# Kernel optimization log

Measured on AMD Instinct MI355X. Metric: run time of the kernel, lower is better.

The kernel has to match this reference:

```python
import jax
import jax.numpy as jnp
import numpy as np
from jax import lax


def setup_inputs() -> dict:
    key = jax.random.key(0)
    k0, k1 = jax.random.split(key)
    B, C, H, W = 8, 256, 96, 96
    FM0 = jax.random.normal(k0, (B, C, H, W), dtype=jnp.float32)
    FM1 = jax.random.normal(k1, (B, C, H, W), dtype=jnp.float32)
    return {"FM0": FM0, "FM1": FM1, "d_max": 4, "stride": 1}


def pointwise_correlation(FM0, FM1, d_max, stride):
    """out[b,h,w,i,j] = sum_c FM0[b,c,h,w] * FM1[b,c,h+(i-d)*s, w+(j-d)*s],
    with zero padding outside FM1's spatial extent."""
    B, C, H, W = FM0.shape
    D = 2 * d_max + 1
    p = d_max * stride
    FM1p = jnp.pad(FM1, ((0, 0), (0, 0), (p, p), (p, p)))
    offs = jnp.arange(D, dtype=jnp.int32) * stride  # start offsets into padded map
    ys, xs = jnp.meshgrid(offs, offs, indexing="ij")
    offsets = jnp.stack([ys.ravel(), xs.ravel()], axis=-1)  # (D*D, 2)

    def step(carry, off):
        sl = lax.dynamic_slice(FM1p, (0, 0, off[0], off[1]), (B, C, H, W))
        corr = jnp.einsum("bchw,bchw->bhw", FM0, sl)
        return carry, corr

    _, out = lax.scan(step, None, offsets)  # (D*D, B, H, W)
    out = out.reshape(D, D, B, H, W).transpose(2, 3, 4, 0, 1)  # (B, H, W, D, D)
    return out


def reference(FM0, FM1, d_max, stride):
    return pointwise_correlation(FM0, FM1, d_max, stride)
```

## Files before the change

### kernel.cpp

```cpp
#include <hip/hip_runtime.h>

#define HH 96
#define WW 96
#define CC 256
#define PLANE (HH * WW)
#define PITCH 20
#define TT 6
#define AROWS (TT * 48)
#define BHROWS (TT + 8)
#define BROWS (BHROWS * 64)
#define ROWS (AROWS + BROWS)
#define LDSN (ROWS * PITCH)
#define NGRP 1184
#define GPT 5
#define NOUT 81
#define NKS 16

typedef __attribute__((ext_vector_type(4))) float f32x4;
typedef __attribute__((ext_vector_type(2))) unsigned int u32x2;
typedef __attribute__((ext_vector_type(4))) short s16x4;

static __device__ __forceinline__ unsigned int pkbf(float x, float y) {
  unsigned int ux = __builtin_bit_cast(unsigned int, x) + 0x8000u;
  unsigned int uy = __builtin_bit_cast(unsigned int, y) + 0x8000u;
  return __builtin_amdgcn_perm(uy, ux, 0x07060302u);
}

static __device__ __forceinline__ f32x4 mfma16x16x16bf16(s16x4 a, s16x4 bm, f32x4 c) {
#if __has_builtin(__builtin_amdgcn_mfma_f32_16x16x16bf16_1k)
  return __builtin_amdgcn_mfma_f32_16x16x16bf16_1k(a, bm, c, 0, 0, 0);
#else
  asm("v_mfma_f32_16x16x16_bf16 %0, %1, %2, %0" : "+v"(c) : "v"(a), "v"(bm));
  return c;
#endif
}

#define BAR_LGKM() asm volatile("s_waitcnt lgkmcnt(0)\n\ts_barrier" ::: "memory")

__global__ __launch_bounds__(1024, 4) void corr_kernel(
    const float* __restrict__ fm0, const float* __restrict__ fm1,
    float* __restrict__ out) {
  __shared__ __align__(16) unsigned short lds[2 * LDSN];

  const int tid = threadIdx.x;
  const int bid = blockIdx.x;
  const int b = bid & 7;
  const int q = bid >> 3;
  const int s = q & 1;
  const int h0 = TT * (q >> 1);

  const int lane = tid & 63;
  const int wv = tid >> 6;
  const int mm = lane & 15;
  const int kg = lane >> 4;

  const size_t boff = (size_t)b * CC * PLANE;

  if (wv >= 12) {
    const int pt = tid - 768;
    const float* gptr[GPT];
    int gdst[GPT];
    unsigned int umask[GPT];
    bool gact[GPT];
    #pragma unroll
    for (int j = 0; j < GPT; ++j) {
      const int g = pt + 256 * j;
      gact[j] = (g < NGRP);
      bool ok;
      if (g < AROWS) {
        const int ar = g / 48, r = g % 48;
        const int cq = r / 12, wq = r - 12 * cq;
        ok = gact[j];
        gdst[j] = (ar * 48 + 4 * wq) * PITCH + 4 * cq;
        gptr[j] = fm0 + boff + (size_t)(4 * cq) * PLANE + (h0 + ar) * WW +
                  (48 * s + 4 * wq);
      } else {
        const int gb = g - AROWS;
        const int ii = gb >> 6, r = gb & 63;
        const int cq = r >> 4, wq = r & 15;
        const int hb = h0 - 4 + ii;
        const int wst = 48 * s - 8 + 4 * wq;
        ok = gact[j] && (hb >= 0) && (hb < HH) && (wst >= 0) && (wst < WW);
        gdst[j] = (AROWS + ii * 64 + 4 * wq) * PITCH + 4 * cq;
        gptr[j] = fm1 + boff + (size_t)(4 * cq) * PLANE +
                  (size_t)(ok ? hb : 0) * WW + (ok ? wst : 0);
      }
      umask[j] = ok ? 0xFFFFFFFFu : 0u;
    }

    f32x4 pre[GPT][4];
    #pragma unroll
    for (int j = 0; j < GPT; ++j)
      #pragma unroll
      for (int cc = 0; cc < 4; ++cc)
        pre[j][cc] = *(const f32x4*)(gptr[j] + (size_t)cc * PLANE);
    #pragma unroll
    for (int j = 0; j < GPT; ++j)
      if (gact[j]) {
        #pragma unroll
        for (int dw = 0; dw < 4; ++dw) {
          u32x2 v;
          v.x = pkbf(pre[j][0][dw], pre[j][1][dw]) & umask[j];
          v.y = pkbf(pre[j][2][dw], pre[j][3][dw]) & umask[j];
          *(u32x2*)&lds[gdst[j] + dw * PITCH] = v;
        }
      }
    #pragma unroll
    for (int j = 0; j < GPT; ++j)
      #pragma unroll
      for (int cc = 0; cc < 4; ++cc)
        pre[j][cc] = *(const f32x4*)(gptr[j] + (size_t)16 * PLANE +
                                     (size_t)cc * PLANE);
    BAR_LGKM();

    #pragma unroll 1
    for (int ks = 0; ks < NKS; ++ks) {
      if (ks < NKS - 1) {
        const int bn = ((ks + 1) & 1) * LDSN;
        const size_t koff = (size_t)((ks + 2) * 16) * PLANE;
        #pragma unroll
        for (int j = 0; j < GPT; ++j) {
          if (gact[j]) {
            #pragma unroll
            for (int dw = 0; dw < 4; ++dw) {
              u32x2 v;
              v.x = pkbf(pre[j][0][dw], pre[j][1][dw]) & umask[j];
              v.y = pkbf(pre[j][2][dw], pre[j][3][dw]) & umask[j];
              *(u32x2*)&lds[bn + gdst[j] + dw * PITCH] = v;
            }
          }
          if (ks < NKS - 2) {
            #pragma unroll
            for (int cc = 0; cc < 4; ++cc)
              pre[j][cc] = *(const f32x4*)(gptr[j] + koff + (size_t)cc * PLANE);
          }
        }
        BAR_LGKM();
      }
    }
  } else {
    const int a = wv >> 1;
    const int u = wv & 1;
    f32x4 acc[9][3];
    #pragma unroll
    for (int i = 0; i < 9; ++i)
      #pragma unroll
      for (int mt = 0; mt < 3; ++mt) acc[i][mt] = f32x4{0.f, 0.f, 0.f, 0.f};

    const int abase = (a * 48 + mm) * PITCH + kg * 4;
    const int bbase = (AROWS + mm) * PITCH + kg * 4;
    asm volatile("s_barrier" ::: "memory");

    #pragma unroll 1
    for (int ks = 0; ks < NKS; ++ks) {
      const int bo = (ks & 1) * LDSN;
      s16x4 af[3];
      #pragma unroll
      for (int mt = 0; mt < 3; ++mt)
        af[mt] = *(const s16x4*)&lds[bo + abase + 16 * mt * PITCH];
      #pragma unroll
      for (int i = 0; i < 9; ++i) {
        const int bb = bo + bbase + (a + i) * 64 * PITCH;
        #pragma unroll
        for (int mt = 0; mt < 3; ++mt) {
          const s16x4 bt = *(const s16x4*)&lds[bb + 16 * (mt + u) * PITCH];
          acc[i][mt] = mfma16x16x16bf16(af[mt], bt, acc[i][mt]);
        }
      }
      if (ks < NKS - 1) BAR_LGKM();
    }

    float* outb = out + ((size_t)b * PLANE + (size_t)(h0 + a) * WW) * NOUT;
    #pragma unroll
    for (int rg = 0; rg < 4; ++rg) {
      const int j = 16 * u + mm - 4 * kg - rg - 4;
      if ((unsigned)j < 9u) {
        #pragma unroll
        for (int i = 0; i < 9; ++i)
          #pragma unroll
          for (int mt = 0; mt < 3; ++mt) {
            const int w = 48 * s + 16 * mt + 4 * kg + rg;
            outb[(size_t)w * NOUT + i * 9 + j] = acc[i][mt][rg];
          }
      }
    }
  }
}

extern "C" void kernel_launch(void* const* d_in, const int* in_sizes, int n_in,
                              void* d_out, int out_size, void* d_ws, size_t ws_size,
                              hipStream_t stream) {
  const float* fm0 = (const float*)d_in[0];
  const float* fm1 = (const float*)d_in[1];
  float* out = (float*)d_out;
  corr_kernel<<<dim3(256), dim3(1024), 0, stream>>>(fm0, fm1, out);
}
```

Baseline: 189.9 us.

## Switch to full-width 3-row tiles with per-channel bf16 LDS staging

Each block now covers 3 output rows across the full width instead of 6 rows over half the width. The FM1 halo becomes 11 rows by 112 columns. The loader warps now fetch 8-byte float pairs per channel and write single bf16 values to LDS, using packed global/LDS offsets in registers and a rolling prefetch depth of 14. LDS is zeroed up front so out-of-range halo columns need no masks. This removes horizontal halo seams but raises redundant vertical halo reads and issues many more small LDS stores.

```diff
diff --git a/kernel.cpp b/kernel.cpp
--- a/kernel.cpp
+++ b/kernel.cpp
@@ -4,26 +4,28 @@
 #define WW 96
 #define CC 256
 #define PLANE (HH * WW)
+#define TT 3
+#define NCH 16
+#define NKS 16
 #define PITCH 20
-#define TT 6
-#define AROWS (TT * 48)
-#define BHROWS (TT + 8)
-#define BROWS (BHROWS * 64)
-#define ROWS (AROWS + BROWS)
+#define AR0WS (TT * WW)
+#define BHR (TT + 8)
+#define BROWS (BHR * 112)
+#define GROW (AR0WS + BROWS)
+#define ROWS (GROW + 2)
 #define LDSN (ROWS * PITCH)
-#define NGRP 1184
-#define GPT 5
 #define NOUT 81
-#define NKS 16
+#define ACH (NCH * TT * 48)
+#define BCH (NCH * BHR * 48)
+#define TCH (ACH + BCH)
+#define DPF 14
 
 typedef __attribute__((ext_vector_type(4))) float f32x4;
-typedef __attribute__((ext_vector_type(2))) unsigned int u32x2;
+typedef __attribute__((ext_vector_type(2))) float f32x2;
 typedef __attribute__((ext_vector_type(4))) short s16x4;
 
-static __device__ __forceinline__ unsigned int pkbf(float x, float y) {
-  unsigned int ux = __builtin_bit_cast(unsigned int, x) + 0x8000u;
-  unsigned int uy = __builtin_bit_cast(unsigned int, y) + 0x8000u;
-  return __builtin_amdgcn_perm(uy, ux, 0x07060302u);
+static __device__ __forceinline__ unsigned short bf1(float x) {
+  return (unsigned short)((__builtin_bit_cast(unsigned int, x) + 0x8000u) >> 16);
 }
 
 static __device__ __forceinline__ f32x4 mfma16x16x16bf16(s16x4 a, s16x4 bm, f32x4 c) {
@@ -40,14 +42,13 @@
 __global__ __launch_bounds__(1024, 4) void corr_kernel(
     const float* __restrict__ fm0, const float* __restrict__ fm1,
     float* __restrict__ out) {
-  __shared__ __align__(16) unsigned short lds[2 * LDSN];
+  __shared__ __align__(16) unsigned short lds16[2 * LDSN];
 
   const int tid = threadIdx.x;
   const int bid = blockIdx.x;
   const int b = bid & 7;
-  const int q = bid >> 3;
-  const int s = q & 1;
-  const int h0 = TT * (q >> 1);
+  const int ht = bid >> 3;
+  const int h0 = TT * ht;
 
   const int lane = tid & 63;
   const int wv = tid >> 6;
@@ -56,90 +57,79 @@
 
   const size_t boff = (size_t)b * CC * PLANE;
 
+  {
+    f32x4* z = (f32x4*)lds16;
+    const int nslots = (2 * LDSN * 2) / 16;
+    #pragma unroll
+    for (int i = 0; i < 8; ++i) {
+      const int idx = tid + 1024 * i;
+      if (idx < nslots) z[idx] = f32x4{0.f, 0.f, 0.f, 0.f};
+    }
+  }
+  BAR_LGKM();
+
   if (wv >= 12) {
     const int pt = tid - 768;
-    const float* gptr[GPT];
-    int gdst[GPT];
-    unsigned int umask[GPT];
-    bool gact[GPT];
+    const float* fA = fm0 + boff;
+    const float* fB = fm1 + boff;
+
+    unsigned int pk[42];
     #pragma unroll
-    for (int j = 0; j < GPT; ++j) {
-      const int g = pt + 256 * j;
-      gact[j] = (g < NGRP);
-      bool ok;
-      if (g < AROWS) {
-        const int ar = g / 48, r = g % 48;
-        const int cq = r / 12, wq = r - 12 * cq;
-        ok = gact[j];
-        gdst[j] = (ar * 48 + 4 * wq) * PITCH + 4 * cq;
-        gptr[j] = fm0 + boff + (size_t)(4 * cq) * PLANE + (h0 + ar) * WW +
-                  (48 * s + 4 * wq);
+    for (int r = 0; r < 42; ++r) {
+      const int id = pt + 256 * r;
+      int goff, lofs;
+      if (id < ACH) {
+        const int c = id / 144;
+        const int r2 = id - 144 * c;
+        const int ar = r2 / 48;
+        const int wq = r2 - 48 * ar;
+        goff = c * PLANE + (h0 + ar) * WW + 2 * wq;
+        lofs = (ar * WW + 2 * wq) * PITCH + c;
       } else {
-        const int gb = g - AROWS;
-        const int ii = gb >> 6, r = gb & 63;
-        const int cq = r >> 4, wq = r & 15;
-        const int hb = h0 - 4 + ii;
-        const int wst = 48 * s - 8 + 4 * wq;
-        ok = gact[j] && (hb >= 0) && (hb < HH) && (wst >= 0) && (wst < WW);
-        gdst[j] = (AROWS + ii * 64 + 4 * wq) * PITCH + 4 * cq;
-        gptr[j] = fm1 + boff + (size_t)(4 * cq) * PLANE +
-                  (size_t)(ok ? hb : 0) * WW + (ok ? wst : 0);
+        const int ib = id - ACH;
+        const int c = ib / 528;
+        const int r2 = ib - 528 * c;
+        const int hbrel = r2 / 48;
+        const int wq = r2 - 48 * hbrel;
+        const int hb = h0 - 4 + hbrel;
+        const bool ok = ((unsigned)hb < (unsigned)HH);
+        goff = c * PLANE + (ok ? hb : 0) * WW + 2 * wq;
+        lofs = ok ? (AR0WS + hbrel * 112 + 8 + 2 * wq) * PITCH + c
+                  : GROW * PITCH + c;
       }
-      umask[j] = ok ? 0xFFFFFFFFu : 0u;
+      pk[r] = ((unsigned int)(goff >> 1) << 15) | (unsigned int)lofs;
     }
 
-    f32x4 pre[GPT][4];
+    f32x2 pre[DPF];
     #pragma unroll
-    for (int j = 0; j < GPT; ++j)
+    for (int p = 0; p < DPF; ++p) {
+      const float* bs = (p < 9) ? fA : fB;
+      pre[p] = *(const f32x2*)(bs + 2 * (size_t)(pk[p] >> 15));
+    }
+
+    #pragma unroll 1
+    for (int ks = 0; ks <= NKS - 1; ++ks) {
+      const int sk = ks;
+      const int bufofs = (sk & 1) * LDSN;
       #pragma unroll
-      for (int cc = 0; cc < 4; ++cc)
-        pre[j][cc] = *(const f32x4*)(gptr[j] + (size_t)cc * PLANE);
-    #pragma unroll
-    for (int j = 0; j < GPT; ++j)
-      if (gact[j]) {
-        #pragma unroll
-        for (int dw = 0; dw < 4; ++dw) {
-          u32x2 v;
-          v.x = pkbf(pre[j][0][dw], pre[j][1][dw]) & umask[j];
-          v.y = pkbf(pre[j][2][dw], pre[j][3][dw]) & umask[j];
-          *(u32x2*)&lds[gdst[j] + dw * PITCH] = v;
+      for (int p = 0; p < 42; ++p) {
+        const f32x2 v = pre[p % DPF];
+        const int lo = (int)(pk[p] & 0x7fffu) + bufofs;
+        lds16[lo] = bf1(v.x);
+        lds16[lo + PITCH] = bf1(v.y);
+        const int q = p + DPF;
+        const int qp = (q >= 42) ? q - 42 : q;
+        const int qs = sk + ((q >= 42) ? 1 : 0);
+        if (qs < NKS) {
+          const float* bs = ((qp < 9) ? fA : fB) + (size_t)qs * NCH * PLANE;
+          pre[qp % DPF] = *(const f32x2*)(bs + 2 * (size_t)(pk[qp] >> 15));
         }
       }
-    #pragma unroll
-    for (int j = 0; j < GPT; ++j)
-      #pragma unroll
-      for (int cc = 0; cc < 4; ++cc)
-        pre[j][cc] = *(const f32x4*)(gptr[j] + (size_t)16 * PLANE +
-                                     (size_t)cc * PLANE);
-    BAR_LGKM();
-
-    #pragma unroll 1
-    for (int ks = 0; ks < NKS; ++ks) {
-      if (ks < NKS - 1) {
-        const int bn = ((ks + 1) & 1) * LDSN;
-        const size_t koff = (size_t)((ks + 2) * 16) * PLANE;
-        #pragma unroll
-        for (int j = 0; j < GPT; ++j) {
-          if (gact[j]) {
-            #pragma unroll
-            for (int dw = 0; dw < 4; ++dw) {
-              u32x2 v;
-              v.x = pkbf(pre[j][0][dw], pre[j][1][dw]) & umask[j];
-              v.y = pkbf(pre[j][2][dw], pre[j][3][dw]) & umask[j];
-              *(u32x2*)&lds[bn + gdst[j] + dw * PITCH] = v;
-            }
-          }
-          if (ks < NKS - 2) {
-            #pragma unroll
-            for (int cc = 0; cc < 4; ++cc)
-              pre[j][cc] = *(const f32x4*)(gptr[j] + koff + (size_t)cc * PLANE);
-          }
-        }
-        BAR_LGKM();
-      }
+      BAR_LGKM();
     }
   } else {
-    const int a = wv >> 1;
+    const int a = wv >> 2;
+    const int mh = (wv >> 1) & 1;
     const int u = wv & 1;
     f32x4 acc[9][3];
     #pragma unroll
@@ -147,9 +137,10 @@
       #pragma unroll
       for (int mt = 0; mt < 3; ++mt) acc[i][mt] = f32x4{0.f, 0.f, 0.f, 0.f};
 
-    const int abase = (a * 48 + mm) * PITCH + kg * 4;
-    const int bbase = (AROWS + mm) * PITCH + kg * 4;
-    asm volatile("s_barrier" ::: "memory");
+    const int abase = (a * WW + 48 * mh + mm) * PITCH + 4 * kg;
+    const int bbase = (AR0WS + 48 * mh + mm) * PITCH + 4 * kg;
+
+    BAR_LGKM();
 
     #pragma unroll 1
     for (int ks = 0; ks < NKS; ++ks) {
@@ -157,13 +148,13 @@
       s16x4 af[3];
       #pragma unroll
       for (int mt = 0; mt < 3; ++mt)
-        af[mt] = *(const s16x4*)&lds[bo + abase + 16 * mt * PITCH];
+        af[mt] = *(const s16x4*)&lds16[bo + abase + 16 * mt * PITCH];
       #pragma unroll
       for (int i = 0; i < 9; ++i) {
-        const int bb = bo + bbase + (a + i) * 64 * PITCH;
+        const int bb = bo + bbase + (a + i) * 112 * PITCH;
         #pragma unroll
         for (int mt = 0; mt < 3; ++mt) {
-          const s16x4 bt = *(const s16x4*)&lds[bb + 16 * (mt + u) * PITCH];
+          const s16x4 bt = *(const s16x4*)&lds16[bb + 16 * (mt + u) * PITCH];
           acc[i][mt] = mfma16x16x16bf16(af[mt], bt, acc[i][mt]);
         }
       }
@@ -179,7 +170,7 @@
         for (int i = 0; i < 9; ++i)
           #pragma unroll
           for (int mt = 0; mt < 3; ++mt) {
-            const int w = 48 * s + 16 * mt + 4 * kg + rg;
+            const int w = 48 * mh + 16 * mt + 4 * kg + rg;
             outb[(size_t)w * NOUT + i * 9 + j] = acc[i][mt][rg];
           }
       }
```

After: 299.1 us. 1.57x slower.
